# Optimization experiments

Hardware: AMD Instinct MI355X
Metric: run time of the kernel (lower is better)

Reference implementation:

```python
import jax, jax.numpy as jnp
import numpy as np

N = 100000   # nodes
R = 4        # relations
E = 200000   # edges per relation
IN = 256
HID = 64
OUT = 64
H = 8        # heads
NEG_SLOPE = 0.2


def setup_inputs() -> dict:
    key = jax.random.key(0)
    ks = jax.random.split(key, 13)
    s = 0.05
    return {
        "x": jax.random.normal(ks[0], (N, IN), jnp.float32),
        "src": jax.random.randint(ks[1], (R, E), 0, N),
        "dst": jax.random.randint(ks[2], (R, E), 0, N),
        "W0": jax.random.normal(ks[3], (R, IN, H * HID), jnp.float32) * s,
        "al0": jax.random.normal(ks[4], (R, H, HID), jnp.float32) * s,
        "ar0": jax.random.normal(ks[5], (R, H, HID), jnp.float32) * s,
        "W1": jax.random.normal(ks[6], (R, H * HID, H * HID), jnp.float32) * s,
        "al1": jax.random.normal(ks[7], (R, H, HID), jnp.float32) * s,
        "ar1": jax.random.normal(ks[8], (R, H, HID), jnp.float32) * s,
        "W2": jax.random.normal(ks[9], (R, H * HID, H * OUT), jnp.float32) * s,
        "al2": jax.random.normal(ks[10], (R, H, OUT), jnp.float32) * s,
        "ar2": jax.random.normal(ks[11], (R, H, OUT), jnp.float32) * s,
    }


def gat_layer(h, src, dst, W, al, ar):
    """Multi-relation GATConv layer; HeteroGraphConv sums ELU'd per-relation outputs.
    h: [N, in]; W: [R, in, H*O]; al/ar: [R, H, O]. Returns [N, H, O]."""
    n = h.shape[0]
    nheads, odim = al.shape[1], al.shape[2]
    acc = jnp.zeros((n, nheads, odim), h.dtype)
    for r in range(W.shape[0]):  # small fixed relation count
        f = (h @ W[r]).reshape(n, nheads, odim)          # [N,H,O]
        el = jnp.sum(f * al[r], axis=-1)                  # [N,H]
        er = jnp.sum(f * ar[r], axis=-1)                  # [N,H]
        s_r, d_r = src[r], dst[r]
        e = jax.nn.leaky_relu(el[s_r] + er[d_r], NEG_SLOPE)  # [E,H]
        # segment softmax over incoming edges per destination node
        m = jax.ops.segment_max(e, d_r, num_segments=n)
        m = jnp.where(jnp.isfinite(m), m, 0.0)
        ex = jnp.exp(e - m[d_r])
        denom = jax.ops.segment_sum(ex, d_r, num_segments=n)
        alpha = ex / (denom[d_r] + 1e-9)                  # [E,H]
        msg = f[s_r] * alpha[:, :, None]                  # [E,H,O]
        out_r = jax.ops.segment_sum(msg, d_r, num_segments=n)  # [N,H,O]
        acc = acc + jax.nn.elu(out_r)
    return acc


def reference(x, src, dst, W0, al0, ar0, W1, al1, ar1, W2, al2, ar2):
    h = gat_layer(x, src, dst, W0, al0, ar0).reshape(N, -1)   # flatten heads
    h = gat_layer(h, src, dst, W1, al1, ar1).reshape(N, -1)   # flatten heads
    h = gat_layer(h, src, dst, W2, al2, ar2).mean(axis=1)     # mean over heads
    return h
```

## Files before the change

kernel.cpp:

```cpp
#include <hip/hip_runtime.h>
#include <hip/hip_bf16.h>
#include <math.h>

#define NNODES 100000
#define NREL 4
#define NEDGE 200000
#define NH 8
#define FDIM 512
#define NMB 782

typedef float f4 __attribute__((ext_vector_type(4)));
typedef __bf16 bf16x8 __attribute__((ext_vector_type(8)));
typedef __bf16 bf16x4 __attribute__((ext_vector_type(4)));

__device__ __forceinline__ float eluf(float v) { return v > 0.f ? v : expm1f(v); }
__device__ __forceinline__ void gload16(const __bf16* g, __bf16* l) {
  __builtin_amdgcn_global_load_lds((const __attribute__((address_space(1))) void*)g,
                                   (__attribute__((address_space(3))) void*)l, 16, 0, 0);
}

__global__ void k_conv(const float* __restrict__ in, __bf16* __restrict__ outp) {
  int i = (blockIdx.x * 256 + threadIdx.x) * 4;
  f4 v = *(const f4*)(in + i);
  bf16x4 o = {(__bf16)v.x, (__bf16)v.y, (__bf16)v.z, (__bf16)v.w};
  *(bf16x4*)(outp + i) = o;
}

__global__ void k_transW(const float* __restrict__ W, __bf16* __restrict__ Wt, int K) {
  __shared__ float tile[32][33];
  int r = blockIdx.z;
  const float* Wr = W + (size_t)r * K * FDIM;
  __bf16* Wtr = Wt + (size_t)r * FDIM * K;
  int k0 = blockIdx.x * 32, n0 = blockIdx.y * 32;
  int tx = threadIdx.x, ty = threadIdx.y;
  for (int i = ty; i < 32; i += 8)
    tile[i][tx] = Wr[(size_t)(k0 + i) * FDIM + n0 + tx];
  __syncthreads();
  for (int i = ty; i < 32; i += 8)
    Wtr[(size_t)(n0 + i) * K + k0 + tx] = (__bf16)tile[tx][i];
}

__global__ __launch_bounds__(256) void k_gemm(const __bf16* __restrict__ A,
                                              const __bf16* __restrict__ BT,
                                              __bf16* __restrict__ C,
                                              const float* __restrict__ al,
                                              const float* __restrict__ ar,
                                              __bf16* __restrict__ el,
                                              __bf16* __restrict__ er, int M, int K) {
  __shared__ alignas(16) __bf16 lds[2][2][128 * 64];
  int t = threadIdx.x, l = t & 63, w = t >> 6;
  int nwg = gridDim.x, q8 = nwg >> 3, r8 = nwg & 7;
  int xx = blockIdx.x & 7, loc = blockIdx.x >> 3;
  int swz = (xx < r8 ? xx * (q8 + 1) : r8 * (q8 + 1) + (xx - r8) * q8) + loc;
  int m0 = (swz >> 2) * 128, n0 = (swz & 3) * 128;
  int wm = (w >> 1) * 64, wn = (w & 1) * 64;
  f4 acc[4][4] = {};

  const __bf16* pSA[4];
  const __bf16* pSB[4];
#pragma unroll
  for (int u = 0; u < 4; u++) {
    int s = t + u * 256;
    int row = s >> 3, c = s & 7;
    int scol = ((c ^ (row & 7)) * 8);
    int ra = m0 + row; if (ra >= M) ra = M - 1;
    pSA[u] = A + (size_t)ra * K + scol;
    pSB[u] = BT + (size_t)(n0 + row) * K + scol;
  }

#define STG(buf, kk)                                          \
  do {                                                        \
    gload16(pSA[0] + (kk), &lds[buf][0][(t) * 8]);            \
    gload16(pSA[1] + (kk), &lds[buf][0][(t + 256) * 8]);      \
    gload16(pSA[2] + (kk), &lds[buf][0][(t + 512) * 8]);      \
    gload16(pSA[3] + (kk), &lds[buf][0][(t + 768) * 8]);      \
    gload16(pSB[0] + (kk), &lds[buf][1][(t) * 8]);            \
    gload16(pSB[1] + (kk), &lds[buf][1][(t + 256) * 8]);      \
    gload16(pSB[2] + (kk), &lds[buf][1][(t + 512) * 8]);      \
    gload16(pSB[3] + (kk), &lds[buf][1][(t + 768) * 8]);      \
  } while (0)

  int rA[4], rB[4];
#pragma unroll
  for (int i = 0; i < 4; i++) {
    int rowA = wm + i * 16 + (l & 15);
    int rowB = wn + i * 16 + (l & 15);
    rA[i] = rowA * 64;
    rB[i] = rowB * 64;
  }
  int ch0 = (l >> 4);

  int nt = K >> 6;
  STG(0, 0);
  for (int kt = 0; kt < nt; kt++) {
    int cb = kt & 1;
    asm volatile("s_waitcnt vmcnt(0)" ::: "memory");
    __builtin_amdgcn_s_barrier();
    __builtin_amdgcn_sched_barrier(0);
    if (kt + 1 < nt) STG(cb ^ 1, (kt + 1) * 64);
    bf16x8 a[4][2], b[4][2];
#pragma unroll
    for (int ks = 0; ks < 2; ks++)
#pragma unroll
      for (int i = 0; i < 4; i++) {
        int ch = ks * 4 + ch0;
        int rowA7 = (rA[i] >> 6) & 7;
        int rowB7 = (rB[i] >> 6) & 7;
        a[i][ks] = *(const bf16x8*)(&lds[cb][0][rA[i] + ((ch ^ rowA7) * 8)]);
        b[i][ks] = *(const bf16x8*)(&lds[cb][1][rB[i] + ((ch ^ rowB7) * 8)]);
      }
#pragma unroll
    for (int ks = 0; ks < 2; ks++)
#pragma unroll
      for (int i = 0; i < 4; i++)
#pragma unroll
        for (int j = 0; j < 4; j++)
          acc[i][j] = __builtin_amdgcn_mfma_f32_16x16x32_bf16(a[i][ks], b[j][ks], acc[i][j], 0, 0, 0);
  }
#undef STG

  int cn = n0 + wn + (l & 15);
  int rbase = m0 + wm + (l >> 4) * 4;
#pragma unroll
  for (int i = 0; i < 4; i++)
#pragma unroll
    for (int q2 = 0; q2 < 4; q2++) {
      int row = rbase + i * 16 + q2;
      if (row < M) {
#pragma unroll
        for (int j = 0; j < 4; j++)
          C[(size_t)row * FDIM + cn + j * 16] = (__bf16)acc[i][j][q2];
      }
    }

  int h = (n0 + wn) >> 6;
  float av[4], bv[4];
#pragma unroll
  for (int j = 0; j < 4; j++) {
    av[j] = al[h * 64 + j * 16 + (l & 15)];
    bv[j] = ar[h * 64 + j * 16 + (l & 15)];
  }
#pragma unroll
  for (int i = 0; i < 4; i++)
#pragma unroll
    for (int q2 = 0; q2 < 4; q2++) {
      float se = acc[i][0][q2] * av[0] + acc[i][1][q2] * av[1] +
                 acc[i][2][q2] * av[2] + acc[i][3][q2] * av[3];
      float sr = acc[i][0][q2] * bv[0] + acc[i][1][q2] * bv[1] +
                 acc[i][2][q2] * bv[2] + acc[i][3][q2] * bv[3];
      se += __shfl_xor(se, 1); se += __shfl_xor(se, 2);
      se += __shfl_xor(se, 4); se += __shfl_xor(se, 8);
      sr += __shfl_xor(sr, 1); sr += __shfl_xor(sr, 2);
      sr += __shfl_xor(sr, 4); sr += __shfl_xor(sr, 8);
      if ((l & 15) == 0) {
        int row = rbase + i * 16 + q2;
        if (row < M) {
          el[row * NH + h] = (__bf16)se;
          er[row * NH + h] = (__bf16)sr;
        }
      }
    }
}

__global__ void k_count(const int* __restrict__ dst, int* __restrict__ deg) {
  int e = blockIdx.x * 256 + threadIdx.x;
  int r = blockIdx.y;
  if (e < NEDGE) {
    int d = dst[(size_t)r * NEDGE + e];
    if ((unsigned)d < (unsigned)NNODES) atomicAdd(&deg[r * NNODES + d], 1);
  }
}

__global__ __launch_bounds__(256) void k_scan_a(const int* __restrict__ in, int* __restrict__ out,
                                                int* __restrict__ bsum, int n) {
  __shared__ int wsums[4];
  int t = threadIdx.x, lane = t & 63, w = t >> 6;
  int base = blockIdx.x * 1024 + t * 4;
  int v0 = base + 0 < n ? in[base + 0] : 0;
  int v1 = base + 1 < n ? in[base + 1] : 0;
  int v2 = base + 2 < n ? in[base + 2] : 0;
  int v3 = base + 3 < n ? in[base + 3] : 0;
  int tot = v0 + v1 + v2 + v3;
  int sc = tot;
#pragma unroll
  for (int off = 1; off < 64; off <<= 1) {
    int u = __shfl_up(sc, off);
    if (lane >= off) sc += u;
  }
  if (lane == 63) wsums[w] = sc;
  __syncthreads();
  int add = 0;
#pragma unroll
  for (int i = 0; i < 4; i++)
    if (i < w) add += wsums[i];
  int excl = add + sc - tot;
  if (base + 0 < n) out[base + 0] = excl;
  if (base + 1 < n) out[base + 1] = excl + v0;
  if (base + 2 < n) out[base + 2] = excl + v0 + v1;
  if (base + 3 < n) out[base + 3] = excl + v0 + v1 + v2;
  if (t == 255) bsum[blockIdx.x] = add + sc;
}

__global__ __launch_bounds__(256) void k_scan_b(int* __restrict__ bsum, int nb) {
  __shared__ int wsums[4];
  int t = threadIdx.x, lane = t & 63, w = t >> 6;
  int i0 = t * 2, i1 = t * 2 + 1;
  int v0 = i0 < nb ? bsum[i0] : 0;
  int v1 = i1 < nb ? bsum[i1] : 0;
  int tot = v0 + v1, sc = tot;
#pragma unroll
  for (int off = 1; off < 64; off <<= 1) {
    int u = __shfl_up(sc, off);
    if (lane >= off) sc += u;
  }
  if (lane == 63) wsums[w] = sc;
  __syncthreads();
  int add = 0;
#pragma unroll
  for (int i = 0; i < 4; i++)
    if (i < w) add += wsums[i];
  int excl = add + sc - tot;
  if (i0 < nb) bsum[i0] = excl;
  if (i1 < nb) bsum[i1] = excl + v0;
}

__global__ void k_scan_c(int* __restrict__ out, const int* __restrict__ bsum, int n) {
  int i = blockIdx.x * 256 + threadIdx.x;
  if (i < n) out[i] += bsum[i >> 10];
}

__global__ void k_scatter(const int* __restrict__ src, const int* __restrict__ dst,
                          const int* __restrict__ ptrf, int* __restrict__ cur,
                          int* __restrict__ csrc) {
  int e = blockIdx.x * 256 + threadIdx.x;
  int r = blockIdx.y;
  if (e >= NEDGE) return;
  int d = dst[(size_t)r * NEDGE + e];
  if ((unsigned)d >= (unsigned)NNODES) return;
  int slot = ptrf[r * NNODES + d] + atomicAdd(&cur[r * NNODES + d], 1);
  if ((unsigned)slot < (unsigned)(NREL * NEDGE))
    csrc[slot] = src[(size_t)r * NEDGE + e];
}

__global__ void k_agg(const __bf16* __restrict__ f, const __bf16* __restrict__ el,
                      const __bf16* __restrict__ er, const int* __restrict__ ptrf,
                      const int* __restrict__ deg, const int* __restrict__ csrc,
                      __bf16* __restrict__ accG, int writeMode) {
  int t = threadIdx.x;
  int l = t & 63;
  int d = blockIdx.x * 4 + (t >> 6);
  int h = l >> 3;
  int cnt = deg[d];
  float res[8] = {0.f, 0.f, 0.f, 0.f, 0.f, 0.f, 0.f, 0.f};
  if (cnt > 0) {
    int start = ptrf[d];
    if (start < 0) start = 0;
    if (start > NREL * NEDGE) start = NREL * NEDGE;
    if (cnt > NREL * NEDGE - start) cnt = NREL * NEDGE - start;
    float erh = (float)er[d * NH + h];
    float a0[8] = {0.f, 0.f, 0.f, 0.f, 0.f, 0.f, 0.f, 0.f};
    float a1[8] = {0.f, 0.f, 0.f, 0.f, 0.f, 0.f, 0.f, 0.f};
    float den = 0.f;
    int j = 0;
    for (; j + 1 < cnt; j += 2) {
      int s0 = csrc[start + j], s1 = csrc[start + j + 1];
      if ((unsigned)s0 >= (unsigned)NNODES) s0 = 0;
      if ((unsigned)s1 >= (unsigned)NNODES) s1 = 0;
      bf16x8 fv0 = *(const bf16x8*)(f + (size_t)s0 * FDIM + l * 8);
      bf16x8 fv1 = *(const bf16x8*)(f + (size_t)s1 * FDIM + l * 8);
      float e0 = (float)el[s0 * NH + h] + erh;
      float e1 = (float)el[s1 * NH + h] + erh;
      e0 = (e0 > 0.f) ? e0 : 0.2f * e0;
      e1 = (e1 > 0.f) ? e1 : 0.2f * e1;
      float ex0 = __expf(e0), ex1 = __expf(e1);
      den += ex0 + ex1;
#pragma unroll
      for (int i = 0; i < 8; i++) {
        a0[i] += ex0 * (float)fv0[i];
        a1[i] += ex1 * (float)fv1[i];
      }
    }
    if (j < cnt) {
      int s0 = csrc[start + j];
      if ((unsigned)s0 >= (unsigned)NNODES) s0 = 0;
      bf16x8 fv0 = *(const bf16x8*)(f + (size_t)s0 * FDIM + l * 8);
      float e0 = (float)el[s0 * NH + h] + erh;
      e0 = (e0 > 0.f) ? e0 : 0.2f * e0;
      float ex0 = __expf(e0);
      den += ex0;
#pragma unroll
      for (int i = 0; i < 8; i++) a0[i] += ex0 * (float)fv0[i];
    }
    float inv = 1.f / (den + 1e-9f);
#pragma unroll
    for (int i = 0; i < 8; i++) res[i] = eluf((a0[i] + a1[i]) * inv);
  } else if (!writeMode) {
    return;
  }
  __bf16* ap = accG + (size_t)d * FDIM + l * 8;
  bf16x8 o;
  if (writeMode) {
#pragma unroll
    for (int i = 0; i < 8; i++) o[i] = (__bf16)res[i];
  } else {
    bf16x8 cv = *(bf16x8*)ap;
#pragma unroll
    for (int i = 0; i < 8; i++) o[i] = (__bf16)((float)cv[i] + res[i]);
  }
  *(bf16x8*)ap = o;
}

__global__ void k_aggm(const __bf16* __restrict__ f, const __bf16* __restrict__ el,
                       const __bf16* __restrict__ er, const int* __restrict__ ptrf,
                       const int* __restrict__ deg, const int* __restrict__ csrc,
                       float* __restrict__ out, int writeMode) {
  int t = threadIdx.x;
  int l = t & 63;
  int d = blockIdx.x * 4 + (t >> 6);
  int h = l >> 3;
  int cnt = deg[d];
  float res[8] = {0.f, 0.f, 0.f, 0.f, 0.f, 0.f, 0.f, 0.f};
  if (cnt > 0) {
    int start = ptrf[d];
    if (start < 0) start = 0;
    if (start > NREL * NEDGE) start = NREL * NEDGE;
    if (cnt > NREL * NEDGE - start) cnt = NREL * NEDGE - start;
    float erh = (float)er[d * NH + h];
    float a0[8] = {0.f, 0.f, 0.f, 0.f, 0.f, 0.f, 0.f, 0.f};
    float a1[8] = {0.f, 0.f, 0.f, 0.f, 0.f, 0.f, 0.f, 0.f};
    float den = 0.f;
    int j = 0;
    for (; j + 1 < cnt; j += 2) {
      int s0 = csrc[start + j], s1 = csrc[start + j + 1];
      if ((unsigned)s0 >= (unsigned)NNODES) s0 = 0;
      if ((unsigned)s1 >= (unsigned)NNODES) s1 = 0;
      bf16x8 fv0 = *(const bf16x8*)(f + (size_t)s0 * FDIM + l * 8);
      bf16x8 fv1 = *(const bf16x8*)(f + (size_t)s1 * FDIM + l * 8);
      float e0 = (float)el[s0 * NH + h] + erh;
      float e1 = (float)el[s1 * NH + h] + erh;
      e0 = (e0 > 0.f) ? e0 : 0.2f * e0;
      e1 = (e1 > 0.f) ? e1 : 0.2f * e1;
      float ex0 = __expf(e0), ex1 = __expf(e1);
      den += ex0 + ex1;
#pragma unroll
      for (int i = 0; i < 8; i++) {
        a0[i] += ex0 * (float)fv0[i];
        a1[i] += ex1 * (float)fv1[i];
      }
    }
    if (j < cnt) {
      int s0 = csrc[start + j];
      if ((unsigned)s0 >= (unsigned)NNODES) s0 = 0;
      bf16x8 fv0 = *(const bf16x8*)(f + (size_t)s0 * FDIM + l * 8);
      float e0 = (float)el[s0 * NH + h] + erh;
      e0 = (e0 > 0.f) ? e0 : 0.2f * e0;
      float ex0 = __expf(e0);
      den += ex0;
#pragma unroll
      for (int i = 0; i < 8; i++) a0[i] += ex0 * (float)fv0[i];
    }
    float inv = 1.f / (den + 1e-9f);
#pragma unroll
    for (int i = 0; i < 8; i++) res[i] = eluf((a0[i] + a1[i]) * inv);
  }
#pragma unroll
  for (int i = 0; i < 8; i++) {
    res[i] += __shfl_xor(res[i], 8);
    res[i] += __shfl_xor(res[i], 16);
    res[i] += __shfl_xor(res[i], 32);
  }
  if (l < 8) {
    float* op = out + (size_t)d * 64 + l * 8;
    f4 v0 = {res[0] * 0.125f, res[1] * 0.125f, res[2] * 0.125f, res[3] * 0.125f};
    f4 v1 = {res[4] * 0.125f, res[5] * 0.125f, res[6] * 0.125f, res[7] * 0.125f};
    if (writeMode) {
      ((f4*)op)[0] = v0;
      ((f4*)op)[1] = v1;
    } else {
      ((f4*)op)[0] += v0;
      ((f4*)op)[1] += v1;
    }
  }
}

extern "C" void kernel_launch(void* const* d_in, const int* in_sizes, int n_in,
                              void* d_out, int out_size, void* d_ws, size_t ws_size,
                              hipStream_t stream) {
  const float* x = (const float*)d_in[0];
  const int* srcp = (const int*)d_in[1];
  const int* dstp = (const int*)d_in[2];
  const float* Wl[3]  = {(const float*)d_in[3], (const float*)d_in[6], (const float*)d_in[9]};
  const float* alp[3] = {(const float*)d_in[4], (const float*)d_in[7], (const float*)d_in[10]};
  const float* arl[3] = {(const float*)d_in[5], (const float*)d_in[8], (const float*)d_in[11]};
  float* out = (float*)d_out;
  (void)in_sizes; (void)n_in; (void)out_size;

  auto rup = [](size_t b) { return (b + 255) & ~(size_t)255; };
  size_t need = 3 * rup((size_t)NNODES * FDIM * 2) +
                2 * rup((size_t)NNODES * NH * 2) +
                rup((size_t)NREL * FDIM * FDIM * 2) +
                2 * rup((size_t)NREL * NNODES * 4) +
                rup((size_t)NREL * NEDGE * 4);
  if (ws_size < need) return;

  char* ws = (char*)d_ws;
  size_t off = 0;
  auto alloc = [&](size_t bytes) -> void* { void* p = ws + off; off += rup(bytes); return p; };
  __bf16* b0   = (__bf16*)alloc((size_t)NNODES * FDIM * 2);
  __bf16* b1   = (__bf16*)alloc((size_t)NNODES * FDIM * 2);
  __bf16* fbuf = (__bf16*)alloc((size_t)NNODES * FDIM * 2);
  __bf16* el   = (__bf16*)alloc((size_t)NNODES * NH * 2);
  __bf16* er   = (__bf16*)alloc((size_t)NNODES * NH * 2);
  __bf16* Wt   = (__bf16*)alloc((size_t)NREL * FDIM * FDIM * 2);
  int* deg  = (int*)alloc((size_t)NREL * NNODES * 4);
  int* ptrf = (int*)alloc((size_t)NREL * NNODES * 4);
  int* csrc = (int*)alloc((size_t)NREL * NEDGE * 4);
  int* cur  = (int*)fbuf;
  int* bsum = (int*)((char*)fbuf + rup((size_t)NREL * NNODES * 4));

  hipMemsetAsync(deg, 0, (size_t)NREL * NNODES * 4, stream);
  hipMemsetAsync(cur, 0, (size_t)NREL * NNODES * 4, stream);
  k_count<<<dim3((NEDGE + 255) / 256, NREL), 256, 0, stream>>>(dstp, deg);
  int ntot = NREL * NNODES;
  int nb1 = (ntot + 1023) / 1024;
  k_scan_a<<<nb1, 256, 0, stream>>>(deg, ptrf, bsum, ntot);
  k_scan_b<<<1, 256, 0, stream>>>(bsum, nb1);
  k_scan_c<<<(ntot + 255) / 256, 256, 0, stream>>>(ptrf, bsum, ntot);
  k_scatter<<<dim3((NEDGE + 255) / 256, NREL), 256, 0, stream>>>(srcp, dstp, ptrf, cur, csrc);

  k_conv<<<(NNODES * 256) / 1024, 256, 0, stream>>>(x, b1);

  int ngrid = NMB * 4;
  for (int L = 0; L < 3; L++) {
    int K = (L == 0) ? 256 : FDIM;
    const __bf16* inb = (L == 1) ? b0 : b1;
    __bf16* outb = (L == 0) ? b0 : b1;
    k_transW<<<dim3(K / 32, 16, NREL), dim3(32, 8), 0, stream>>>(Wl[L], Wt, K);
    for (int r = 0; r < NREL; r++) {
      k_gemm<<<ngrid, 256, 0, stream>>>(inb, Wt + (size_t)r * FDIM * K, fbuf,
                                        alp[L] + (size_t)r * 512,
                                        arl[L] + (size_t)r * 512,
                                        el, er, NNODES, K);
      if (L < 2)
        k_agg<<<NNODES / 4, 256, 0, stream>>>(fbuf, el, er, ptrf + (size_t)r * NNODES,
                                              deg + (size_t)r * NNODES, csrc, outb,
                                              r == 0 ? 1 : 0);
      else
        k_aggm<<<NNODES / 4, 256, 0, stream>>>(fbuf, el, er, ptrf + (size_t)r * NNODES,
                                               deg + (size_t)r * NNODES, csrc, out,
                                               r == 0 ? 1 : 0);
    }
  }
}
```

Measured before the change: 1.868 ms.

## Store GEMM output in permuted column order for vectorized bf16x4 stores

The GEMM epilogue now writes four adjacent bf16 values per row with one 8-byte store instead of four scattered 2-byte stores, which permutes the column order within each 64-wide head. To keep results correct, the weight transpose for later layers permutes the K dimension to match the permuted activation layout. The final-layer output store un-permutes columns with scalar stores. This trades wider epilogue stores for scattered scalar stores in the last aggregation kernel.

```diff
diff --git a/kernel.cpp b/kernel.cpp
--- a/kernel.cpp
+++ b/kernel.cpp
@@ -26,7 +26,8 @@
   *(bf16x4*)(outp + i) = o;
 }
 
-__global__ void k_transW(const float* __restrict__ W, __bf16* __restrict__ Wt, int K) {
+__global__ void k_transW(const float* __restrict__ W, __bf16* __restrict__ Wt, int K,
+                         int permK) {
   __shared__ float tile[32][33];
   int r = blockIdx.z;
   const float* Wr = W + (size_t)r * K * FDIM;
@@ -36,8 +37,10 @@
   for (int i = ty; i < 32; i += 8)
     tile[i][tx] = Wr[(size_t)(k0 + i) * FDIM + n0 + tx];
   __syncthreads();
+  int kp = k0 + tx;
+  int kd = permK ? ((kp & ~63) | ((kp & 15) << 2) | ((kp >> 4) & 3)) : kp;
   for (int i = ty; i < 32; i += 8)
-    Wtr[(size_t)(n0 + i) * K + k0 + tx] = (__bf16)tile[tx][i];
+    Wtr[(size_t)(n0 + i) * K + kd] = (__bf16)tile[tx][i];
 }
 
 __global__ __launch_bounds__(256) void k_gemm(const __bf16* __restrict__ A,
@@ -83,10 +86,8 @@
   int rA[4], rB[4];
 #pragma unroll
   for (int i = 0; i < 4; i++) {
-    int rowA = wm + i * 16 + (l & 15);
-    int rowB = wn + i * 16 + (l & 15);
-    rA[i] = rowA * 64;
-    rB[i] = rowB * 64;
+    rA[i] = (wm + i * 16 + (l & 15)) * 64;
+    rB[i] = (wn + i * 16 + (l & 15)) * 64;
   }
   int ch0 = (l >> 4);
 
@@ -119,17 +120,17 @@
   }
 #undef STG
 
-  int cn = n0 + wn + (l & 15);
   int rbase = m0 + wm + (l >> 4) * 4;
+  int cbase = n0 + wn + (l & 15) * 4;
 #pragma unroll
   for (int i = 0; i < 4; i++)
 #pragma unroll
     for (int q2 = 0; q2 < 4; q2++) {
       int row = rbase + i * 16 + q2;
       if (row < M) {
-#pragma unroll
-        for (int j = 0; j < 4; j++)
-          C[(size_t)row * FDIM + cn + j * 16] = (__bf16)acc[i][j][q2];
+        bf16x4 o = {(__bf16)acc[i][0][q2], (__bf16)acc[i][1][q2],
+                    (__bf16)acc[i][2][q2], (__bf16)acc[i][3][q2]};
+        *(bf16x4*)(&C[(size_t)row * FDIM + cbase]) = o;
       }
     }
 
@@ -370,15 +371,13 @@
     res[i] += __shfl_xor(res[i], 32);
   }
   if (l < 8) {
-    float* op = out + (size_t)d * 64 + l * 8;
-    f4 v0 = {res[0] * 0.125f, res[1] * 0.125f, res[2] * 0.125f, res[3] * 0.125f};
-    f4 v1 = {res[4] * 0.125f, res[5] * 0.125f, res[6] * 0.125f, res[7] * 0.125f};
-    if (writeMode) {
-      ((f4*)op)[0] = v0;
-      ((f4*)op)[1] = v1;
-    } else {
-      ((f4*)op)[0] += v0;
-      ((f4*)op)[1] += v1;
+#pragma unroll
+    for (int i = 0; i < 8; i++) {
+      int sw = l * 8 + i;
+      int p = (sw >> 2) + (sw & 3) * 16;
+      float v = res[i] * 0.125f;
+      if (writeMode) out[(size_t)d * 64 + p] = v;
+      else           out[(size_t)d * 64 + p] += v;
     }
   }
 }
@@ -435,7 +434,7 @@
     int K = (L == 0) ? 256 : FDIM;
     const __bf16* inb = (L == 1) ? b0 : b1;
     __bf16* outb = (L == 0) ? b0 : b1;
-    k_transW<<<dim3(K / 32, 16, NREL), dim3(32, 8), 0, stream>>>(Wl[L], Wt, K);
+    k_transW<<<dim3(K / 32, 16, NREL), dim3(32, 8), 0, stream>>>(Wl[L], Wt, K, L > 0 ? 1 : 0);
     for (int r = 0; r < NREL; r++) {
       k_gemm<<<ngrid, 256, 0, stream>>>(inb, Wt + (size_t)r * FDIM * K, fbuf,
                                         alp[L] + (size_t)r * 512,
```

New measurement: 1.877 ms. About the same (+0.5%).
